# Optimization experiments

Hardware: AMD Instinct MI355X
Metric: run time of the kernel (lower is better)

## Reference

```python
import jax, jax.numpy as jnp
import numpy as np

N_HEADS = 8
D_EMBED = 512
D_CROSS = 768
D_HEAD = D_EMBED // N_HEADS


def setup_inputs() -> dict:
    key = jax.random.key(0)
    ks = jax.random.split(key, 12)
    B, SQ, SKV = 8, 4096, 77
    s_e = 1.0 / np.sqrt(D_EMBED)
    s_c = 1.0 / np.sqrt(D_CROSS)
    return {
        "latent": jax.random.normal(ks[0], (B, SQ, D_EMBED), jnp.float32),
        "context": jax.random.normal(ks[1], (B, SKV, D_CROSS), jnp.float32),
        "wq": jax.random.normal(ks[2], (D_EMBED, D_EMBED), jnp.float32) * s_e,
        "bq": jax.random.normal(ks[3], (D_EMBED,), jnp.float32) * 0.01,
        "wk": jax.random.normal(ks[4], (D_CROSS, D_EMBED), jnp.float32) * s_c,
        "bk": jax.random.normal(ks[5], (D_EMBED,), jnp.float32) * 0.01,
        "wv": jax.random.normal(ks[6], (D_CROSS, D_EMBED), jnp.float32) * s_c,
        "bv": jax.random.normal(ks[7], (D_EMBED,), jnp.float32) * 0.01,
        "wo": jax.random.normal(ks[8], (D_EMBED, D_EMBED), jnp.float32) * s_e,
        "bo": jax.random.normal(ks[9], (D_EMBED,), jnp.float32) * 0.01,
    }


def reference(latent, context, wq, bq, wk, bk, wv, bv, wo, bo):
    B, SQ, _ = latent.shape
    SKV = context.shape[1]
    # projections; weights stored as (in, out)
    q = latent @ wq + bq                     # [B, SQ, D_EMBED]
    k = context @ wk + bk                    # [B, SKV, D_EMBED]
    v = context @ wv + bv                    # [B, SKV, D_EMBED]
    # split heads -> [B, H, S, Dh]
    q = q.reshape(B, SQ, N_HEADS, D_HEAD).transpose(0, 2, 1, 3)
    k = k.reshape(B, SKV, N_HEADS, D_HEAD).transpose(0, 2, 1, 3)
    v = v.reshape(B, SKV, N_HEADS, D_HEAD).transpose(0, 2, 1, 3)
    scale = 1.0 / np.sqrt(D_HEAD).astype(np.float32)
    w = jnp.einsum("bhqd,bhkd->bhqk", q, k) * scale  # [B, H, SQ, SKV]
    w = jax.nn.softmax(w, axis=-1)
    out = jnp.einsum("bhqk,bhkd->bhqd", w, v)        # [B, H, SQ, Dh]
    out = out.transpose(0, 2, 1, 3).reshape(B, SQ, D_EMBED)
    return out @ wo + bo
```

## Files before the change

### kernel.cpp

```cpp
#include <hip/hip_runtime.h>


typedef __attribute__((ext_vector_type(8))) __bf16 bf16x8;
typedef __attribute__((ext_vector_type(4))) float f32x4;

#define DEVI static __device__ __forceinline__

typedef __attribute__((address_space(3))) void lds_void_t;
typedef const __attribute__((address_space(1))) void gbl_void_t;
#define GLDS16(gsrc, ldst) \
  __builtin_amdgcn_global_load_lds((gbl_void_t*)(gsrc), (lds_void_t*)(ldst), 16, 0, 0)

DEVI unsigned short f2bf(float f) {
  unsigned int u = __float_as_uint(f);
  u += 0x7FFFu + ((u >> 16) & 1u);
  return (unsigned short)(u >> 16);
}

DEVI unsigned int cvt_pk_bf16(float lo, float hi) {
  unsigned int r;
  asm("v_cvt_pk_bf16_f32 %0, %1, %2" : "=v"(r) : "v"(lo), "v"(hi));
  return r;
}

DEVI bf16x8 cvt8(float4 a, float4 b) {
  uint4 u;
  u.x = cvt_pk_bf16(a.x, a.y);
  u.y = cvt_pk_bf16(a.z, a.w);
  u.z = cvt_pk_bf16(b.x, b.y);
  u.w = cvt_pk_bf16(b.z, b.w);
  return *(bf16x8*)&u;
}

__global__ __launch_bounds__(256) void wtrans_all_kernel(
    const float* __restrict__ wq, const float* __restrict__ wk,
    const float* __restrict__ wv, const float* __restrict__ wo,
    unsigned short* __restrict__ wqT, unsigned short* __restrict__ wkT,
    unsigned short* __restrict__ wvT, unsigned short* __restrict__ woT,
    uint4* __restrict__ zbuf) {
  __shared__ float tile[32][33];
  int bid = blockIdx.x;
  int tid = threadIdx.x;
  if (bid >= 1280) {
    uint4 z = {0u, 0u, 0u, 0u};
    zbuf[(size_t)(bid - 1280) * 256 + tid] = z;
    return;
  }
  const float* in;
  unsigned short* out;
  int K, r;
  if (bid < 256)       { in = wq; out = wqT; K = 512; r = bid; }
  else if (bid < 640)  { in = wk; out = wkT; K = 768; r = bid - 256; }
  else if (bid < 1024) { in = wv; out = wvT; K = 768; r = bid - 640; }
  else                 { in = wo; out = woT; K = 512; r = bid - 1024; }
  int n0 = (r & 15) * 32, k0 = (r >> 4) * 32;
  int tx = tid & 31, ty = tid >> 5;
#pragma unroll
  for (int j = 0; j < 4; ++j)
    tile[ty * 4 + j][tx] = in[(size_t)(k0 + ty * 4 + j) * 512 + n0 + tx];
  __syncthreads();
#pragma unroll
  for (int j = 0; j < 4; ++j)
    out[(size_t)(n0 + ty * 4 + j) * K + k0 + tx] = f2bf(tile[tx][ty * 4 + j]);
}

__global__ __launch_bounds__(256) void kv_proj_kernel(const float* __restrict__ ctx,
                                                      const unsigned short* __restrict__ wkT,
                                                      const unsigned short* __restrict__ wvT,
                                                      const float* __restrict__ bk,
                                                      const float* __restrict__ bv,
                                                      unsigned short* __restrict__ Kp,
                                                      unsigned short* __restrict__ Vt) {
  __shared__ __align__(16) unsigned short As[64][40];
  __shared__ __align__(16) unsigned short Bs[64][40];
  int bid = blockIdx.x;
  int sel = bid / 80;
  int rem = bid % 80;
  int mt = rem / 8, nt = rem % 8;
  const unsigned short* wT = sel ? wvT : wkT;
  const float* bias = sel ? bv : bk;
  int tid = threadIdx.x;
  int l = tid & 63, w = tid >> 6;
  int lr = l & 15, lg = l >> 4;

  f32x4 acc[4] = {};
  for (int k0 = 0; k0 < 768; k0 += 32) {
#pragma unroll
    for (int it = 0; it < 2; ++it) {
      int idx4 = it * 256 + tid;
      int r = idx4 >> 3, q4 = idx4 & 7;
      int m = mt * 64 + r;
      float4 v = {0.f, 0.f, 0.f, 0.f};
      if (m < 616) v = *(const float4*)(ctx + (size_t)m * 768 + k0 + q4 * 4);
      ushort4 o;
      o.x = f2bf(v.x); o.y = f2bf(v.y); o.z = f2bf(v.z); o.w = f2bf(v.w);
      *(ushort4*)&As[r][q4 * 4] = o;
    }
    {
      int c = tid >> 2, q8 = tid & 3;
      *(uint4*)&Bs[c][q8 * 8] =
          *(const uint4*)(wT + (size_t)(nt * 64 + c) * 768 + k0 + q8 * 8);
    }
    __syncthreads();
    bf16x8 a = *(const bf16x8*)&As[w * 16 + lr][lg * 8];
#pragma unroll
    for (int n = 0; n < 4; ++n) {
      bf16x8 bb = *(const bf16x8*)&Bs[n * 16 + lr][lg * 8];
      acc[n] = __builtin_amdgcn_mfma_f32_16x16x32_bf16(a, bb, acc[n], 0, 0, 0);
    }
    __syncthreads();
  }
#pragma unroll
  for (int n = 0; n < 4; ++n) {
#pragma unroll
    for (int reg = 0; reg < 4; ++reg) {
      int m = mt * 64 + w * 16 + lg * 4 + reg;
      if (m < 616) {
        int bI = m / 77, s = m % 77;
        int col = nt * 64 + n * 16 + lr;
        int h = col >> 6, d = col & 63;
        float v = acc[n][reg] + bias[col];
        if (sel == 0)
          Kp[(((size_t)(bI * 8 + h)) * 80 + s) * 64 + d] = f2bf(v);
        else
          Vt[(((size_t)(bI * 8 + h)) * 64 + d) * 96 + s] = f2bf(v);
      }
    }
  }
}

#define QSTEP(t, AO)                                                          \
  {                                                                           \
    if ((t) < 15)                                                             \
      asm volatile("s_waitcnt vmcnt(4)" ::: "memory");                        \
    else                                                                      \
      asm volatile("s_waitcnt vmcnt(0)" ::: "memory");                        \
    __builtin_amdgcn_s_barrier();                                             \
    __builtin_amdgcn_sched_barrier(0);                                        \
    const float* Af = (const float*)(smem + (AO));                            \
    const unsigned short* Bf = smem + 16384;                                  \
    const int swA = lr & 7;                                                   \
    const int swB = (lr >> 1) & 3;                                            \
    float4 ax[4], ay[4];                                                      \
    bf16x8 bv8[4];                                                            \
    _Pragma("unroll") for (int m = 0; m < 4; ++m) {                           \
      ax[m] = *(const float4*)&Af[(wr + m * 16 + lr) * 32 +                   \
                                  ((2 * lg) ^ swA) * 4];                      \
      ay[m] = *(const float4*)&Af[(wr + m * 16 + lr) * 32 +                   \
                                  ((2 * lg + 1) ^ swA) * 4];                  \
    }                                                                         \
    _Pragma("unroll") for (int n = 0; n < 4; ++n)                             \
        bv8[n] = *(const bf16x8*)&Bf[(wc + n * 16 + lr) * 32 +                \
                                     (lg ^ swB) * 8];                         \
    asm volatile("s_waitcnt lgkmcnt(0)" ::: "memory");                        \
    __builtin_amdgcn_sched_barrier(0);                                        \
    __builtin_amdgcn_s_barrier();                                             \
    if ((t) <= 14) {                                                          \
      int nk1 = ((t) + 1) * 32;                                               \
      GLDS16(gB + nk1, smem + 16384 + w * 1024);                              \
      GLDS16(gB + nk1 + 16 * 512, smem + 16384 + w * 1024 + 512);             \
    }                                                                         \
    if ((t) <= 13) {                                                          \
      int nk2 = ((t) + 2) * 32;                                               \
      _Pragma("unroll") for (int i = 0; i < 4; ++i)                           \
          GLDS16(gA32 + nk2 + i * 4096, smem + (AO) + w * 2048 + i * 512);    \
    }                                                                         \
    bf16x8 af[4];                                                             \
    _Pragma("unroll") for (int m = 0; m < 4; ++m) af[m] = cvt8(ax[m], ay[m]); \
    _Pragma("unroll") for (int m = 0; m < 4; ++m)                             \
        _Pragma("unroll") for (int n = 0; n < 4; ++n)                         \
            acc[m][n] = __builtin_amdgcn_mfma_f32_16x16x32_bf16(              \
                af[m], bv8[n], acc[m][n], 0, 0, 0);                           \
  }

__global__ __launch_bounds__(256, 4) void qproj_attn_kernel(
    const float* __restrict__ A32, const unsigned short* __restrict__ BT,
    const float* __restrict__ bias, const unsigned short* __restrict__ Kp,
    const unsigned short* __restrict__ Vt, unsigned short* __restrict__ Oq) {
  __shared__ __align__(16) unsigned short smem[20480];

  int bid = ((blockIdx.x & 7) << 7) | (blockIdx.x >> 3);
  size_t mbase = (size_t)(bid >> 2) * 128;
  int nbase = (bid & 3) * 128;
  int tid = threadIdx.x;
  int l = tid & 63, w = tid >> 6;
  int lr = l & 15, lg = l >> 4;
  int wr = (w >> 1) * 64, wc = (w & 1) * 64;

  const float* gA32 =
      A32 + (mbase + w * 32 + (l >> 3)) * 512 + (((l & 7) ^ (l >> 3))) * 4;
  const unsigned short* gB = BT + (size_t)(nbase + w * 32 + (l >> 2)) * 512 +
                             (((l & 3) ^ ((l >> 3) & 3))) * 8;

#pragma unroll
  for (int i = 0; i < 4; ++i) GLDS16(gA32 + i * 4096, smem + w * 2048 + i * 512);
  GLDS16(gB, smem + 16384 + w * 1024);
  GLDS16(gB + 16 * 512, smem + 16384 + w * 1024 + 512);
#pragma unroll
  for (int i = 0; i < 4; ++i)
    GLDS16(gA32 + 32 + i * 4096, smem + 8192 + w * 2048 + i * 512);

  f32x4 acc[4][4] = {};
#pragma unroll 1
  for (int t = 0; t < 16; t += 2) {
    QSTEP(t, 0);
    QSTEP(t + 1, 8192);
  }

  unsigned short* Qme = smem + w * (64 * 72);
  float bb[4];
#pragma unroll
  for (int n = 0; n < 4; ++n) bb[n] = bias[nbase + wc + n * 16 + lr];
#pragma unroll
  for (int m = 0; m < 4; ++m)
#pragma unroll
    for (int n = 0; n < 4; ++n)
#pragma unroll
      for (int reg = 0; reg < 4; ++reg)
        Qme[(m * 16 + lg * 4 + reg) * 72 + n * 16 + lr] = f2bf(acc[m][n][reg] + bb[n]);

  bf16x8 qf[4][2];
#pragma unroll
  for (int rg = 0; rg < 4; ++rg) {
    qf[rg][0] = *(const bf16x8*)&Qme[(rg * 16 + lr) * 72 + lg * 8];
    qf[rg][1] = *(const bf16x8*)&Qme[(rg * 16 + lr) * 72 + 32 + lg * 8];
  }

  unsigned short* Pme = Qme;
  unsigned short* Ome = Qme + 1664;
  for (int z = l; z < 256; z += 64) Pme[(z >> 4) * 104 + 80 + (z & 15)] = 0;

  int b = (int)(mbase >> 12);
  int h = (bid & 3) * 2 + (w & 1);
  const unsigned short* Kph = Kp + (size_t)(b * 8 + h) * (80 * 64);
  const unsigned short* Vth = Vt + (size_t)(b * 8 + h) * (64 * 96);

  const float C = 0.125f * 1.44269504088896f;

  auto QK = [&](int rg, f32x4* s) {
#pragma unroll
    for (int t = 0; t < 5; ++t) {
      const unsigned short* kr = Kph + (t * 16 + lr) * 64 + lg * 8;
      bf16x8 k0 = *(const bf16x8*)kr;
      bf16x8 k1 = *(const bf16x8*)(kr + 32);
      s[t] = __builtin_amdgcn_mfma_f32_16x16x32_bf16(qf[rg][0], k0, s[t], 0, 0, 0);
      s[t] = __builtin_amdgcn_mfma_f32_16x16x32_bf16(qf[rg][1], k1, s[t], 0, 0, 0);
    }
    if (lr >= 13) {
      s[4][0] = -1e30f; s[4][1] = -1e30f; s[4][2] = -1e30f; s[4][3] = -1e30f;
    }
  };

  f32x4 sc[5] = {};
  QK(0, sc);
#pragma unroll
  for (int rg = 0; rg < 4; ++rg) {
    float mx[4];
#pragma unroll
    for (int r = 0; r < 4; ++r)
      mx[r] = fmaxf(fmaxf(fmaxf(sc[0][r], sc[1][r]), fmaxf(sc[2][r], sc[3][r])), sc[4][r]);
#pragma unroll
    for (int d = 1; d < 16; d <<= 1)
#pragma unroll
      for (int r = 0; r < 4; ++r) mx[r] = fmaxf(mx[r], __shfl_xor(mx[r], d, 64));
    float p[5][4];
#pragma unroll
    for (int t = 0; t < 5; ++t)
#pragma unroll
      for (int r = 0; r < 4; ++r) p[t][r] = exp2f((sc[t][r] - mx[r]) * C);
#pragma unroll
    for (int t = 0; t < 5; ++t)
#pragma unroll
      for (int r = 0; r < 4; ++r)
        Pme[(lg * 4 + r) * 104 + t * 16 + lr] = f2bf(p[t][r]);

    float sm[4];
#pragma unroll
    for (int r = 0; r < 4; ++r)
      sm[r] = p[0][r] + p[1][r] + p[2][r] + p[3][r] + p[4][r];
#pragma unroll
    for (int d = 1; d < 16; d <<= 1)
#pragma unroll
      for (int r = 0; r < 4; ++r) sm[r] += __shfl_xor(sm[r], d, 64);
    float rs[4];
#pragma unroll
    for (int r = 0; r < 4; ++r) rs[r] = 1.0f / sm[r];

    f32x4 sn[5] = {};
    if (rg < 3) QK(rg + 1, sn);

    bf16x8 ap[3];
#pragma unroll
    for (int c = 0; c < 3; ++c) ap[c] = *(const bf16x8*)&Pme[lr * 104 + c * 32 + lg * 8];
#pragma unroll
    for (int ct = 0; ct < 4; ++ct) {
      f32x4 o = {};
#pragma unroll
      for (int c = 0; c < 3; ++c) {
        bf16x8 vv = *(const bf16x8*)(Vth + (size_t)(ct * 16 + lr) * 96 + c * 32 + lg * 8);
        o = __builtin_amdgcn_mfma_f32_16x16x32_bf16(ap[c], vv, o, 0, 0, 0);
      }
#pragma unroll
      for (int reg = 0; reg < 4; ++reg)
        Ome[(lg * 4 + reg) * 72 + ct * 16 + lr] = f2bf(o[reg] * rs[reg]);
    }
    {
      size_t rowbase = mbase + wr + rg * 16;
      int r8 = l >> 3, c8 = (l & 7) * 8;
      uint4 v0 = *(const uint4*)&Ome[r8 * 72 + c8];
      uint4 v1 = *(const uint4*)&Ome[(r8 + 8) * 72 + c8];
      *(uint4*)&Oq[(rowbase + r8) * 512 + nbase + wc + c8] = v0;
      *(uint4*)&Oq[(rowbase + r8 + 8) * 512 + nbase + wc + c8] = v1;
    }
#pragma unroll
    for (int t = 0; t < 5; ++t) sc[t] = sn[t];
  }
}

#define KSTEP(t, boff)                                                        \
  {                                                                           \
    if ((t) < 15)                                                             \
      asm volatile("s_waitcnt vmcnt(4)" ::: "memory");                        \
    else                                                                      \
      asm volatile("s_waitcnt vmcnt(0)" ::: "memory");                        \
    __builtin_amdgcn_s_barrier();                                             \
    __builtin_amdgcn_sched_barrier(0);                                        \
    const unsigned short* bufA = smem + (boff);                               \
    const unsigned short* bufB = bufA + 4096;                                 \
    const int swB = (lr >> 1) & 3;                                            \
    bf16x8 af[4], bv8[4];                                                     \
    _Pragma("unroll") for (int m = 0; m < 4; ++m)                             \
        af[m] = *(const bf16x8*)&bufA[(wr + m * 16 + lr) * 32 +               \
                                      (lg ^ swB) * 8];                        \
    _Pragma("unroll") for (int n = 0; n < 4; ++n)                             \
        bv8[n] = *(const bf16x8*)&bufB[(wc + n * 16 + lr) * 32 +              \
                                       (lg ^ swB) * 8];                       \
    asm volatile("s_waitcnt lgkmcnt(0)" ::: "memory");                        \
    __builtin_amdgcn_sched_barrier(0);                                        \
    __builtin_amdgcn_s_barrier();                                             \
    if ((t) <= 13) {                                                          \
      int nk = ((t) + 2) * 32;                                                \
      GLDS16(gA + nk, smem + (boff) + w * 1024);                              \
      GLDS16(gA + nk + 16 * 512, smem + (boff) + w * 1024 + 512);             \
      GLDS16(gB + nk, smem + (boff) + 4096 + w * 1024);                       \
      GLDS16(gB + nk + 16 * 512, smem + (boff) + 4096 + w * 1024 + 512);      \
    }                                                                         \
    _Pragma("unroll") for (int m = 0; m < 4; ++m)                             \
        _Pragma("unroll") for (int n = 0; n < 4; ++n)                         \
            acc[m][n] = __builtin_amdgcn_mfma_f32_16x16x32_bf16(              \
                af[m], bv8[n], acc[m][n], 0, 0, 0);                           \
  }

__global__ __launch_bounds__(256) void gemm512_glds_kernel(
    const unsigned short* __restrict__ A, const unsigned short* __restrict__ BT,
    const float* __restrict__ bias, float* __restrict__ Out) {
  __shared__ __align__(16) unsigned short smem[16384];
  int bid = ((blockIdx.x & 7) << 7) | (blockIdx.x >> 3);
  size_t mbase = (size_t)(bid >> 2) * 128;
  int nbase = (bid & 3) * 128;
  int tid = threadIdx.x;
  int l = tid & 63, w = tid >> 6;
  int lr = l & 15, lg = l >> 4;
  int wr = (w >> 1) * 64, wc = (w & 1) * 64;

  const unsigned short* gA = A + (mbase + w * 32 + (l >> 2)) * 512 +
                             (((l & 3) ^ ((l >> 3) & 3))) * 8;
  const unsigned short* gB = BT + (size_t)(nbase + w * 32 + (l >> 2)) * 512 +
                             (((l & 3) ^ ((l >> 3) & 3))) * 8;

  GLDS16(gA, smem + w * 1024);
  GLDS16(gA + 16 * 512, smem + w * 1024 + 512);
  GLDS16(gB, smem + 4096 + w * 1024);
  GLDS16(gB + 16 * 512, smem + 4096 + w * 1024 + 512);
  GLDS16(gA + 32, smem + 8192 + w * 1024);
  GLDS16(gA + 32 + 16 * 512, smem + 8192 + w * 1024 + 512);
  GLDS16(gB + 32, smem + 12288 + w * 1024);
  GLDS16(gB + 32 + 16 * 512, smem + 12288 + w * 1024 + 512);

  f32x4 acc[4][4] = {};
#pragma unroll 1
  for (int t = 0; t < 16; t += 2) {
    KSTEP(t, 0);
    KSTEP(t + 1, 8192);
  }

#pragma unroll
  for (int m = 0; m < 4; ++m) {
#pragma unroll
    for (int n = 0; n < 4; ++n) {
#pragma unroll
      for (int reg = 0; reg < 4; ++reg) {
        size_t row = mbase + wr + m * 16 + lg * 4 + reg;
        int col = nbase + wc + n * 16 + lr;
        Out[row * 512 + col] = acc[m][n][reg] + bias[col];
      }
    }
  }
}

static const size_t OFF_Q   = 0;
static const size_t OFF_KP  = 33554432;
static const size_t OFF_VT  = OFF_KP + 655360;
static const size_t OFF_WQT = OFF_VT + 786432;
static const size_t OFF_WKT = OFF_WQT + 524288;
static const size_t OFF_WVT = OFF_WKT + 786432;
static const size_t OFF_WOT = OFF_WVT + 786432;
static const size_t WS_NEEDED = OFF_WOT + 524288;

extern "C" void kernel_launch(void* const* d_in, const int* in_sizes, int n_in,
                              void* d_out, int out_size, void* d_ws, size_t ws_size,
                              hipStream_t stream) {
  (void)in_sizes; (void)n_in; (void)out_size;
  if (ws_size < WS_NEEDED) return;

  const float* latent  = (const float*)d_in[0];
  const float* context = (const float*)d_in[1];
  const float* wq = (const float*)d_in[2];
  const float* bq = (const float*)d_in[3];
  const float* wk = (const float*)d_in[4];
  const float* bk = (const float*)d_in[5];
  const float* wv = (const float*)d_in[6];
  const float* bv = (const float*)d_in[7];
  const float* wo = (const float*)d_in[8];
  const float* bo = (const float*)d_in[9];
  float* out = (float*)d_out;

  char* ws = (char*)d_ws;
  unsigned short* wsQ = (unsigned short*)(ws + OFF_Q);
  unsigned short* Kp  = (unsigned short*)(ws + OFF_KP);
  unsigned short* Vt  = (unsigned short*)(ws + OFF_VT);
  unsigned short* wqT = (unsigned short*)(ws + OFF_WQT);
  unsigned short* wkT = (unsigned short*)(ws + OFF_WKT);
  unsigned short* wvT = (unsigned short*)(ws + OFF_WVT);
  unsigned short* woT = (unsigned short*)(ws + OFF_WOT);

  wtrans_all_kernel<<<1280 + 352, 256, 0, stream>>>(
      wq, wk, wv, wo, wqT, wkT, wvT, woT, (uint4*)(ws + OFF_KP));
  kv_proj_kernel<<<160, 256, 0, stream>>>(context, wkT, wvT, bk, bv, Kp, Vt);
  qproj_attn_kernel<<<1024, 256, 0, stream>>>(latent, wqT, bq, Kp, Vt, wsQ);
  gemm512_glds_kernel<<<1024, 256, 0, stream>>>(wsQ, woT, bo, out);
}
```

Measured before the change: 114.0 us.

## Transpose QK MFMA and pass softmax probabilities via shuffles instead of LDS

Swaps the operands of the QK MFMA so each lane holds scores for a single query row. Row max and sum then reduce over two cross-lane shuffles instead of four, and normalization is folded into the probabilities before packing them to bf16. The P tile is built in registers with lane shuffles, removing the LDS round trip for P and the LDS staging for O. The output is now written directly with scattered 2-byte global stores, which may coalesce worse than the previous 16-byte stores.

```diff
diff --git a/kernel.cpp b/kernel.cpp
--- a/kernel.cpp
+++ b/kernel.cpp
@@ -226,10 +226,6 @@
     qf[rg][1] = *(const bf16x8*)&Qme[(rg * 16 + lr) * 72 + 32 + lg * 8];
   }
 
-  unsigned short* Pme = Qme;
-  unsigned short* Ome = Qme + 1664;
-  for (int z = l; z < 256; z += 64) Pme[(z >> 4) * 104 + 80 + (z & 15)] = 0;
-
   int b = (int)(mbase >> 12);
   int h = (bid & 3) * 2 + (w & 1);
   const unsigned short* Kph = Kp + (size_t)(b * 8 + h) * (80 * 64);
@@ -243,55 +239,72 @@
       const unsigned short* kr = Kph + (t * 16 + lr) * 64 + lg * 8;
       bf16x8 k0 = *(const bf16x8*)kr;
       bf16x8 k1 = *(const bf16x8*)(kr + 32);
-      s[t] = __builtin_amdgcn_mfma_f32_16x16x32_bf16(qf[rg][0], k0, s[t], 0, 0, 0);
-      s[t] = __builtin_amdgcn_mfma_f32_16x16x32_bf16(qf[rg][1], k1, s[t], 0, 0, 0);
-    }
-    if (lr >= 13) {
-      s[4][0] = -1e30f; s[4][1] = -1e30f; s[4][2] = -1e30f; s[4][3] = -1e30f;
+      s[t] = __builtin_amdgcn_mfma_f32_16x16x32_bf16(k0, qf[rg][0], s[t], 0, 0, 0);
+      s[t] = __builtin_amdgcn_mfma_f32_16x16x32_bf16(k1, qf[rg][1], s[t], 0, 0, 0);
     }
   };
+
+  const int srcLo = 32 * (lg & 1) + lr;
+  const int srcHi = srcLo + 16;
+  const int selHi = lg >> 1;
 
   f32x4 sc[5] = {};
   QK(0, sc);
 #pragma unroll
   for (int rg = 0; rg < 4; ++rg) {
-    float mx[4];
-#pragma unroll
-    for (int r = 0; r < 4; ++r)
-      mx[r] = fmaxf(fmaxf(fmaxf(sc[0][r], sc[1][r]), fmaxf(sc[2][r], sc[3][r])), sc[4][r]);
-#pragma unroll
-    for (int d = 1; d < 16; d <<= 1)
-#pragma unroll
-      for (int r = 0; r < 4; ++r) mx[r] = fmaxf(mx[r], __shfl_xor(mx[r], d, 64));
+    float mx = sc[0][0];
+#pragma unroll
+    for (int t = 0; t < 5; ++t)
+#pragma unroll
+      for (int r = 0; r < 4; ++r) mx = fmaxf(mx, sc[t][r]);
+    mx = fmaxf(mx, __shfl_xor(mx, 16, 64));
+    mx = fmaxf(mx, __shfl_xor(mx, 32, 64));
     float p[5][4];
 #pragma unroll
     for (int t = 0; t < 5; ++t)
 #pragma unroll
-      for (int r = 0; r < 4; ++r) p[t][r] = exp2f((sc[t][r] - mx[r]) * C);
+      for (int r = 0; r < 4; ++r) p[t][r] = exp2f((sc[t][r] - mx) * C);
+    if (lg == 3) { p[4][1] = 0.f; p[4][2] = 0.f; p[4][3] = 0.f; }
+    float sm = 0.f;
 #pragma unroll
     for (int t = 0; t < 5; ++t)
 #pragma unroll
-      for (int r = 0; r < 4; ++r)
-        Pme[(lg * 4 + r) * 104 + t * 16 + lr] = f2bf(p[t][r]);
-
-    float sm[4];
-#pragma unroll
-    for (int r = 0; r < 4; ++r)
-      sm[r] = p[0][r] + p[1][r] + p[2][r] + p[3][r] + p[4][r];
-#pragma unroll
-    for (int d = 1; d < 16; d <<= 1)
-#pragma unroll
-      for (int r = 0; r < 4; ++r) sm[r] += __shfl_xor(sm[r], d, 64);
-    float rs[4];
-#pragma unroll
-    for (int r = 0; r < 4; ++r) rs[r] = 1.0f / sm[r];
+      for (int r = 0; r < 4; ++r) sm += p[t][r];
+    sm += __shfl_xor(sm, 16, 64);
+    sm += __shfl_xor(sm, 32, 64);
+    float rs = 1.0f / sm;
+    unsigned int pk[5][2];
+#pragma unroll
+    for (int t = 0; t < 5; ++t) {
+      pk[t][0] = cvt_pk_bf16(p[t][0] * rs, p[t][1] * rs);
+      pk[t][1] = cvt_pk_bf16(p[t][2] * rs, p[t][3] * rs);
+    }
 
     f32x4 sn[5] = {};
     if (rg < 3) QK(rg + 1, sn);
 
     bf16x8 ap[3];
 #pragma unroll
-    for (int c = 0; c < 3; ++c) ap[c] = *(const bf16x8*)&Pme[lr * 104 + c * 32 + lg * 8];
+    for (int c = 0; c < 3; ++c) {
+      unsigned int a0 = __shfl((int)pk[2 * c][0], srcLo, 64);
+      unsigned int a1 = __shfl((int)pk[2 * c][1], srcLo, 64);
+      unsigned int a2 = __shfl((int)pk[2 * c][0], srcHi, 64);
+      unsigned int a3 = __shfl((int)pk[2 * c][1], srcHi, 64);
+      unsigned int b0 = 0, b1 = 0, b2 = 0, b3 = 0;
+      if (c < 2) {
+        b0 = __shfl((int)pk[2 * c + 1][0], srcLo, 64);
+        b1 = __shfl((int)pk[2 * c + 1][1], srcLo, 64);
+        b2 = __shfl((int)pk[2 * c + 1][0], srcHi, 64);
+        b3 = __shfl((int)pk[2 * c + 1][1], srcHi, 64);
+      }
+      uint4 u;
+      u.x = selHi ? b0 : a0;
+      u.y = selHi ? b1 : a1;
+      u.z = selHi ? b2 : a2;
+      u.w = selHi ? b3 : a3;
+      ap[c] = *(bf16x8*)&u;
+    }
+
 #pragma unroll
     for (int ct = 0; ct < 4; ++ct) {
       f32x4 o = {};
@@ -302,15 +315,8 @@
       }
 #pragma unroll
       for (int reg = 0; reg < 4; ++reg)
-        Ome[(lg * 4 + reg) * 72 + ct * 16 + lr] = f2bf(o[reg] * rs[reg]);
-    }
-    {
-      size_t rowbase = mbase + wr + rg * 16;
-      int r8 = l >> 3, c8 = (l & 7) * 8;
-      uint4 v0 = *(const uint4*)&Ome[r8 * 72 + c8];
-      uint4 v1 = *(const uint4*)&Ome[(r8 + 8) * 72 + c8];
-      *(uint4*)&Oq[(rowbase + r8) * 512 + nbase + wc + c8] = v0;
-      *(uint4*)&Oq[(rowbase + r8 + 8) * 512 + nbase + wc + c8] = v1;
+        Oq[(mbase + wr + rg * 16 + lg * 4 + reg) * 512 + nbase + wc + ct * 16 + lr] =
+            f2bf(o[reg]);
     }
 #pragma unroll
     for (int t = 0; t < 5; ++t) sc[t] = sn[t];
```

Result: faster. 109.7 us (-3.7%).
